# Kernel tuning notes

Measured on AMD Instinct MI355X. Metric: run time of the kernel, lower is better.

The kernel has to match this reference:

```python
import jax, jax.numpy as jnp
import numpy as np

B, ISIZE, HSIZE = 256, 256, 512
CLIPVAL = 2.0

def _linear(x, W, b):
    # torch nn.Linear: y = x @ W.T + b, W is [out, in]
    return x @ W.T + b

def setup_inputs() -> dict:
    key = jax.random.key(0)
    ks = jax.random.split(key, 24)
    d = {}
    d['inputs'] = jax.random.normal(ks[0], (B, ISIZE), jnp.float32)
    d['h0'] = jax.random.normal(ks[1], (B, HSIZE), jnp.float32) * 0.1
    d['c0'] = jax.random.normal(ks[2], (B, HSIZE), jnp.float32) * 0.1
    d['hebb'] = jax.random.normal(ks[3], (B, HSIZE, HSIZE), jnp.float32) * 0.01
    d['w'] = 0.02 * jax.random.uniform(ks[4], (HSIZE, HSIZE), jnp.float32) - 0.01
    d['alpha'] = 0.0001 * jax.random.uniform(ks[5], (1, 1, HSIZE), jnp.float32)
    scale_h = 1.0 / np.sqrt(HSIZE)
    scale_i = 1.0 / np.sqrt(ISIZE)
    d['h2f_w'] = jax.random.uniform(ks[6], (HSIZE, HSIZE), jnp.float32, -scale_h, scale_h)
    d['h2f_b'] = jax.random.uniform(ks[7], (HSIZE,), jnp.float32, -scale_h, scale_h)
    d['h2i_w'] = jax.random.uniform(ks[8], (HSIZE, HSIZE), jnp.float32, -scale_h, scale_h)
    d['h2i_b'] = jax.random.uniform(ks[9], (HSIZE,), jnp.float32, -scale_h, scale_h)
    d['h2opt_w'] = jax.random.uniform(ks[10], (HSIZE, HSIZE), jnp.float32, -scale_h, scale_h)
    d['h2opt_b'] = jax.random.uniform(ks[11], (HSIZE,), jnp.float32, -scale_h, scale_h)
    d['x2f_w'] = jax.random.uniform(ks[12], (HSIZE, ISIZE), jnp.float32, -scale_i, scale_i)
    d['x2f_b'] = jax.random.uniform(ks[13], (HSIZE,), jnp.float32, -scale_i, scale_i)
    d['x2i_w'] = jax.random.uniform(ks[14], (HSIZE, ISIZE), jnp.float32, -scale_i, scale_i)
    d['x2i_b'] = jax.random.uniform(ks[15], (HSIZE,), jnp.float32, -scale_i, scale_i)
    d['x2opt_w'] = jax.random.uniform(ks[16], (HSIZE, ISIZE), jnp.float32, -scale_i, scale_i)
    d['x2opt_b'] = jax.random.uniform(ks[17], (HSIZE,), jnp.float32, -scale_i, scale_i)
    d['x2c_w'] = jax.random.uniform(ks[18], (HSIZE, ISIZE), jnp.float32, -scale_i, scale_i)
    d['x2c_b'] = jax.random.uniform(ks[19], (HSIZE,), jnp.float32, -scale_i, scale_i)
    d['h2mod_w'] = jax.random.uniform(ks[20], (1, HSIZE), jnp.float32, -scale_h, scale_h)
    d['h2mod_b'] = jax.random.uniform(ks[21], (1,), jnp.float32, -scale_h, scale_h)
    d['modfanout_w'] = jax.random.uniform(ks[22], (HSIZE, 1), jnp.float32, -1.0, 1.0)
    d['modfanout_b'] = jax.random.uniform(ks[23], (HSIZE,), jnp.float32, -1.0, 1.0)
    return d

def reference(inputs, h0, c0, hebb, w, alpha,
              h2f_w, h2f_b, h2i_w, h2i_b, h2opt_w, h2opt_b,
              x2f_w, x2f_b, x2i_w, x2i_b, x2opt_w, x2opt_b, x2c_w, x2c_b,
              h2mod_w, h2mod_b, modfanout_w, modfanout_b):
    # gates
    fgt = jax.nn.sigmoid(_linear(inputs, x2f_w, x2f_b) + _linear(h0, h2f_w, h2f_b))
    ipt = jax.nn.sigmoid(_linear(inputs, x2i_w, x2i_b) + _linear(h0, h2i_w, h2i_b))
    opt = jax.nn.sigmoid(_linear(inputs, x2opt_w, x2opt_b) + _linear(h0, h2opt_w, h2opt_b))
    # plastic recurrent matmul: h [B,h] x (w + alpha*hebb) [B,h,h]
    M = w[None, :, :] + alpha * hebb  # [B, h, h]
    h2coutput = jnp.einsum('bh,bhk->bk', h0, M)
    inputstocell = jnp.tanh(_linear(inputs, x2c_w, x2c_b) + h2coutput)
    cell = fgt * c0 + ipt * inputstocell
    hactiv = opt * jnp.tanh(cell)
    # Hebbian outer product (hebboutput='i2c')
    deltahebb = h0[:, :, None] * inputstocell[:, None, :]  # [B, h, h]
    # modulation: modultype='modplasth2mod', modulout='fanout'
    m = jnp.tanh(_linear(hactiv, h2mod_w, h2mod_b))  # [B, 1]
    fan = m[:, 0][:, None] * modfanout_w[:, 0][None, :] + modfanout_b[None, :]  # [B, h]
    myeta = fan[:, None, :]  # [B, 1, h]
    # cliptype='clip'
    hebb_new = jnp.clip(hebb + myeta * deltahebb, -CLIPVAL, CLIPVAL)
    return hactiv, cell, hebb_new
```

## Files before the change

kernel.cpp:

```cpp
#include <hip/hip_runtime.h>
#include <math.h>

#define BATCH 256
#define ISZ 256
#define H 512
#define BH (BATCH * H)
#define CLIPV 2.0f

typedef float f4_t __attribute__((ext_vector_type(4)));

__device__ __forceinline__ float sigmoidf_(float x) { return 1.0f / (1.0f + expf(-x)); }
__device__ __forceinline__ f4_t nt_load4(const f4_t* p) { return __builtin_nontemporal_load(p); }
__device__ __forceinline__ void nt_store4(f4_t* p, f4_t v) { __builtin_nontemporal_store(v, p); }

#define BT 64
#define KT 32
#define LDSP (BT + 4)
#define NGEMM 256
#define NEIN  1024

__global__ __launch_bounds__(256) void gemms_einsum(
    const float* __restrict__ x, const float* __restrict__ h0,
    const float* __restrict__ x2f_w, const float* __restrict__ x2f_b,
    const float* __restrict__ h2f_w, const float* __restrict__ h2f_b,
    const float* __restrict__ x2i_w, const float* __restrict__ x2i_b,
    const float* __restrict__ h2i_w, const float* __restrict__ h2i_b,
    const float* __restrict__ x2o_w, const float* __restrict__ x2o_b,
    const float* __restrict__ h2o_w, const float* __restrict__ h2o_b,
    const float* __restrict__ x2c_w, const float* __restrict__ x2c_b,
    const float* __restrict__ w,
    const float* __restrict__ hebb,
    float* __restrict__ pre, float* __restrict__ hbpart)
{
  __shared__ __align__(16) float As[KT][LDSP];
  __shared__ __align__(16) float Bs[KT][LDSP];
  __shared__ float h0s[128];
  __shared__ f4_t redv[128];

  const int bid = blockIdx.x;
  const int t   = threadIdx.x;

  if (bid >= NGEMM) {
    const int e    = bid - NGEMM;
    const int b    = e >> 2;
    const int seg  = e & 3;
    const int col  = t & 127;
    const int half = t >> 7;
    if (t < 128) h0s[t] = h0[b * H + seg * 128 + t];
    __syncthreads();
    const f4_t* hb4 = (const f4_t*)hebb +
        (size_t)(b * H + seg * 128 + half * 64) * (H / 4) + col;
    f4_t acc = {0.f, 0.f, 0.f, 0.f};
    #pragma unroll 8
    for (int h = 0; h < 64; ++h) {
      acc += h0s[half * 64 + h] * hb4[(size_t)h * 128];
    }
    if (half == 1) redv[col] = acc;
    __syncthreads();
    if (half == 0) {
      acc += redv[col];
      ((f4_t*)hbpart)[(size_t)(b * 4 + seg) * 128 + col] = acc;
    }
    return;
  }

  const int ch  = bid >> 5;
  const int rem = bid & 31;
  const int n0  = (rem & 7) * BT;
  const int m0  = (rem >> 3) * BT;
  const int tx = t & 15, ty = t >> 4;

  const float* A; const float* Bm; int lda, K; bool kmajor = true;
  const float* b1 = nullptr; const float* b2 = nullptr;
  switch (ch) {
    case 0: A = x;  lda = ISZ; K = ISZ; Bm = x2f_w; b1 = x2f_b; b2 = h2f_b; break;
    case 1: A = h0; lda = H;   K = H;   Bm = h2f_w; break;
    case 2: A = x;  lda = ISZ; K = ISZ; Bm = x2i_w; b1 = x2i_b; b2 = h2i_b; break;
    case 3: A = h0; lda = H;   K = H;   Bm = h2i_w; break;
    case 4: A = x;  lda = ISZ; K = ISZ; Bm = x2o_w; b1 = x2o_b; b2 = h2o_b; break;
    case 5: A = h0; lda = H;   K = H;   Bm = h2o_w; break;
    case 6: A = x;  lda = ISZ; K = ISZ; Bm = x2c_w; b1 = x2c_b; break;
    default: A = h0; lda = H;  K = H;   Bm = w; kmajor = false; break;
  }

  float acc[4][4] = {{0.0f}};

  for (int kk0 = 0; kk0 < K; kk0 += KT) {
    #pragma unroll
    for (int i = 0; i < 2; ++i) {
      int l = i * 256 + t;
      int r = l >> 3, c = l & 7;
      float4 v = *(const float4*)&A[(size_t)(m0 + r) * lda + kk0 + c * 4];
      As[c * 4 + 0][r] = v.x; As[c * 4 + 1][r] = v.y;
      As[c * 4 + 2][r] = v.z; As[c * 4 + 3][r] = v.w;
    }
    if (kmajor) {
      #pragma unroll
      for (int i = 0; i < 2; ++i) {
        int l = i * 256 + t;
        int n = l >> 3, c = l & 7;
        float4 v = *(const float4*)&Bm[(size_t)(n0 + n) * K + kk0 + c * 4];
        Bs[c * 4 + 0][n] = v.x; Bs[c * 4 + 1][n] = v.y;
        Bs[c * 4 + 2][n] = v.z; Bs[c * 4 + 3][n] = v.w;
      }
    } else {
      #pragma unroll
      for (int i = 0; i < 2; ++i) {
        int l = i * 256 + t;
        int j = l >> 4, c = l & 15;
        float4 v = *(const float4*)&Bm[(size_t)(kk0 + j) * H + n0 + c * 4];
        *(float4*)&Bs[j][c * 4] = v;
      }
    }
    __syncthreads();
    #pragma unroll
    for (int j = 0; j < KT; ++j) {
      float4 a  = *(const float4*)&As[j][ty * 4];
      float4 bv = *(const float4*)&Bs[j][tx * 4];
      float av[4] = {a.x, a.y, a.z, a.w};
      float bw[4] = {bv.x, bv.y, bv.z, bv.w};
      #pragma unroll
      for (int r = 0; r < 4; ++r)
        #pragma unroll
        for (int c = 0; c < 4; ++c)
          acc[r][c] += av[r] * bw[c];
    }
    __syncthreads();
  }

  float bias[4];
  #pragma unroll
  for (int c = 0; c < 4; ++c) {
    int n = n0 + tx * 4 + c;
    float bv = 0.0f;
    if (b1) bv += b1[n];
    if (b2) bv += b2[n];
    bias[c] = bv;
  }
  float* outc = pre + (size_t)ch * BH;
  #pragma unroll
  for (int r = 0; r < 4; ++r) {
    int m = m0 + ty * 4 + r;
    float4 o;
    o.x = acc[r][0] + bias[0];
    o.y = acc[r][1] + bias[1];
    o.z = acc[r][2] + bias[2];
    o.w = acc[r][3] + bias[3];
    *(float4*)&outc[(size_t)m * H + n0 + tx * 4] = o;
  }
}

__global__ __launch_bounds__(256) void fuse_mod(
    const float* __restrict__ pre, const float* __restrict__ hbpart,
    const float* __restrict__ c0, const float* __restrict__ alpha,
    const float* __restrict__ h2mod_w, const float* __restrict__ h2mod_b,
    const float* __restrict__ mfo_w, const float* __restrict__ mfo_b,
    float* __restrict__ out, float* __restrict__ eta)
{
  const int b = blockIdx.x, t = threadIdx.x;
  float ha[2], itcv[2];
  #pragma unroll
  for (int u = 0; u < 2; ++u) {
    const int k   = t + u * 256;
    const int idx = b * H + k;
    float hb = 0.0f;
    #pragma unroll
    for (int s = 0; s < 4; ++s) hb += hbpart[(size_t)(b * 4 + s) * H + k];
    float h2c = pre[(size_t)7 * BH + idx] + alpha[k] * hb;
    float it  = tanhf(pre[(size_t)6 * BH + idx] + h2c);
    float f = sigmoidf_(pre[idx]                + pre[(size_t)1 * BH + idx]);
    float i = sigmoidf_(pre[(size_t)2 * BH + idx] + pre[(size_t)3 * BH + idx]);
    float o = sigmoidf_(pre[(size_t)4 * BH + idx] + pre[(size_t)5 * BH + idx]);
    float cell = f * c0[idx] + i * it;
    float h = o * tanhf(cell);
    out[idx] = h;
    out[BH + idx] = cell;
    ha[u] = h; itcv[u] = it;
  }
  float s = ha[0] * h2mod_w[t] + ha[1] * h2mod_w[t + 256];
  #pragma unroll
  for (int off = 32; off > 0; off >>= 1) s += __shfl_down(s, off, 64);
  __shared__ float red[4];
  __shared__ float mm;
  if ((t & 63) == 0) red[t >> 6] = s;
  __syncthreads();
  if (t == 0) mm = tanhf(red[0] + red[1] + red[2] + red[3] + h2mod_b[0]);
  __syncthreads();
  float m = mm;
  #pragma unroll
  for (int u = 0; u < 2; ++u) {
    const int k = t + u * 256;
    eta[b * H + k] = (m * mfo_w[k] + mfo_b[k]) * itcv[u];
  }
}

__global__ __launch_bounds__(256) void hebb_update(
    const float* __restrict__ hebb, const float* __restrict__ h0,
    const float* __restrict__ eta, float* __restrict__ out)
{
  const size_t g = (size_t)(gridDim.x - 1 - blockIdx.x) * 256 + threadIdx.x;
  f4_t v = nt_load4((const f4_t*)hebb + g);
  const int k4  = (int)(g & 127);
  const int row = (int)(g >> 7);
  const int b   = row >> 9;
  f4_t e = ((const f4_t*)eta)[(b << 7) + k4];
  float s = h0[row];
  f4_t r;
  r.x = fminf(fmaxf(v.x + s * e.x, -CLIPV), CLIPV);
  r.y = fminf(fmaxf(v.y + s * e.y, -CLIPV), CLIPV);
  r.z = fminf(fmaxf(v.z + s * e.z, -CLIPV), CLIPV);
  r.w = fminf(fmaxf(v.w + s * e.w, -CLIPV), CLIPV);
  nt_store4((f4_t*)out + (size_t)(2 * BH / 4) + g, r);
}

extern "C" void kernel_launch(void* const* d_in, const int* in_sizes, int n_in,
                              void* d_out, int out_size, void* d_ws, size_t ws_size,
                              hipStream_t stream) {
  const float* x       = (const float*)d_in[0];
  const float* h0      = (const float*)d_in[1];
  const float* c0      = (const float*)d_in[2];
  const float* hebb    = (const float*)d_in[3];
  const float* w       = (const float*)d_in[4];
  const float* alpha   = (const float*)d_in[5];
  const float* h2f_w   = (const float*)d_in[6];
  const float* h2f_b   = (const float*)d_in[7];
  const float* h2i_w   = (const float*)d_in[8];
  const float* h2i_b   = (const float*)d_in[9];
  const float* h2o_w   = (const float*)d_in[10];
  const float* h2o_b   = (const float*)d_in[11];
  const float* x2f_w   = (const float*)d_in[12];
  const float* x2f_b   = (const float*)d_in[13];
  const float* x2i_w   = (const float*)d_in[14];
  const float* x2i_b   = (const float*)d_in[15];
  const float* x2o_w   = (const float*)d_in[16];
  const float* x2o_b   = (const float*)d_in[17];
  const float* x2c_w   = (const float*)d_in[18];
  const float* x2c_b   = (const float*)d_in[19];
  const float* h2mod_w = (const float*)d_in[20];
  const float* h2mod_b = (const float*)d_in[21];
  const float* mfo_w   = (const float*)d_in[22];
  const float* mfo_b   = (const float*)d_in[23];

  float* out = (float*)d_out;
  float* ws  = (float*)d_ws;

  float* pre    = ws;
  float* hbpart = pre + (size_t)8 * BH;
  float* eta    = hbpart + (size_t)BATCH * 4 * H;

  gemms_einsum<<<NGEMM + NEIN, 256, 0, stream>>>(
      x, h0, x2f_w, x2f_b, h2f_w, h2f_b, x2i_w, x2i_b, h2i_w, h2i_b,
      x2o_w, x2o_b, h2o_w, h2o_b, x2c_w, x2c_b, w, hebb, pre, hbpart);

  fuse_mod<<<BATCH, 256, 0, stream>>>(
      pre, hbpart, c0, alpha, h2mod_w, h2mod_b, mfo_w, mfo_b, out, eta);

  hebb_update<<<(BH * (H / 4)) / 256, 256, 0, stream>>>(hebb, h0, eta, out);
}
```

Baseline: 541.1 us.

## Fuse hebb einsum, gate math and hebb update into one per-batch kernel

Moves the plastic einsum out of the GEMM kernel into a per-batch kernel that computes h0·hebb, the gate nonlinearities, the modulation and the clipped Hebbian update in one launch. The aim is to reread each batch's 1 MB hebb slice right after reducing over it, so the second read may hit L2/MALL instead of HBM, and to drop the hbpart and eta workspace round trips plus one launch. The cost is only 256 blocks of 512 threads doing all of the 256 MB hebb traffic, so there may not be enough bytes in flight to saturate HBM bandwidth. The einsum also no longer overlaps with the GEMM blocks.

```diff
diff --git a/kernel.cpp b/kernel.cpp
--- a/kernel.cpp
+++ b/kernel.cpp
@@ -7,19 +7,16 @@
 #define BH (BATCH * H)
 #define CLIPV 2.0f
 
-typedef float f4_t __attribute__((ext_vector_type(4)));
-
-__device__ __forceinline__ float sigmoidf_(float x) { return 1.0f / (1.0f + expf(-x)); }
-__device__ __forceinline__ f4_t nt_load4(const f4_t* p) { return __builtin_nontemporal_load(p); }
-__device__ __forceinline__ void nt_store4(f4_t* p, f4_t v) { __builtin_nontemporal_store(v, p); }
-
 #define BT 64
 #define KT 32
 #define LDSP (BT + 4)
-#define NGEMM 256
-#define NEIN  1024
-
-__global__ __launch_bounds__(256) void gemms_einsum(
+
+typedef float f4_t __attribute__((ext_vector_type(4)));
+
+__device__ __forceinline__ float sigmoidf_(float x) { return 1.0f / (1.0f + expf(-x)); }
+__device__ __forceinline__ void nt_store4(f4_t* p, f4_t v) { __builtin_nontemporal_store(v, p); }
+
+__global__ __launch_bounds__(256) void gemms(
     const float* __restrict__ x, const float* __restrict__ h0,
     const float* __restrict__ x2f_w, const float* __restrict__ x2f_b,
     const float* __restrict__ h2f_w, const float* __restrict__ h2f_b,
@@ -29,41 +26,13 @@
     const float* __restrict__ h2o_w, const float* __restrict__ h2o_b,
     const float* __restrict__ x2c_w, const float* __restrict__ x2c_b,
     const float* __restrict__ w,
-    const float* __restrict__ hebb,
-    float* __restrict__ pre, float* __restrict__ hbpart)
+    float* __restrict__ pre)
 {
   __shared__ __align__(16) float As[KT][LDSP];
   __shared__ __align__(16) float Bs[KT][LDSP];
-  __shared__ float h0s[128];
-  __shared__ f4_t redv[128];
 
   const int bid = blockIdx.x;
   const int t   = threadIdx.x;
-
-  if (bid >= NGEMM) {
-    const int e    = bid - NGEMM;
-    const int b    = e >> 2;
-    const int seg  = e & 3;
-    const int col  = t & 127;
-    const int half = t >> 7;
-    if (t < 128) h0s[t] = h0[b * H + seg * 128 + t];
-    __syncthreads();
-    const f4_t* hb4 = (const f4_t*)hebb +
-        (size_t)(b * H + seg * 128 + half * 64) * (H / 4) + col;
-    f4_t acc = {0.f, 0.f, 0.f, 0.f};
-    #pragma unroll 8
-    for (int h = 0; h < 64; ++h) {
-      acc += h0s[half * 64 + h] * hb4[(size_t)h * 128];
-    }
-    if (half == 1) redv[col] = acc;
-    __syncthreads();
-    if (half == 0) {
-      acc += redv[col];
-      ((f4_t*)hbpart)[(size_t)(b * 4 + seg) * 128 + col] = acc;
-    }
-    return;
-  }
-
   const int ch  = bid >> 5;
   const int rem = bid & 31;
   const int n0  = (rem & 7) * BT;
@@ -84,7 +53,6 @@
   }
 
   float acc[4][4] = {{0.0f}};
-
   for (int kk0 = 0; kk0 < K; kk0 += KT) {
     #pragma unroll
     for (int i = 0; i < 2; ++i) {
@@ -150,67 +118,79 @@
   }
 }
 
-__global__ __launch_bounds__(256) void fuse_mod(
-    const float* __restrict__ pre, const float* __restrict__ hbpart,
-    const float* __restrict__ c0, const float* __restrict__ alpha,
+__global__ __launch_bounds__(512) void batch_fused(
+    const float* __restrict__ pre, const float* __restrict__ hebb,
+    const float* __restrict__ h0, const float* __restrict__ c0,
+    const float* __restrict__ alpha,
     const float* __restrict__ h2mod_w, const float* __restrict__ h2mod_b,
     const float* __restrict__ mfo_w, const float* __restrict__ mfo_b,
-    float* __restrict__ out, float* __restrict__ eta)
+    float* __restrict__ out)
 {
-  const int b = blockIdx.x, t = threadIdx.x;
-  float ha[2], itcv[2];
-  #pragma unroll
-  for (int u = 0; u < 2; ++u) {
-    const int k   = t + u * 256;
-    const int idx = b * H + k;
-    float hb = 0.0f;
-    #pragma unroll
-    for (int s = 0; s < 4; ++s) hb += hbpart[(size_t)(b * 4 + s) * H + k];
-    float h2c = pre[(size_t)7 * BH + idx] + alpha[k] * hb;
-    float it  = tanhf(pre[(size_t)6 * BH + idx] + h2c);
-    float f = sigmoidf_(pre[idx]                + pre[(size_t)1 * BH + idx]);
-    float i = sigmoidf_(pre[(size_t)2 * BH + idx] + pre[(size_t)3 * BH + idx]);
-    float o = sigmoidf_(pre[(size_t)4 * BH + idx] + pre[(size_t)5 * BH + idx]);
-    float cell = f * c0[idx] + i * it;
-    float h = o * tanhf(cell);
-    out[idx] = h;
-    out[BH + idx] = cell;
-    ha[u] = h; itcv[u] = it;
-  }
-  float s = ha[0] * h2mod_w[t] + ha[1] * h2mod_w[t + 256];
+  __shared__ float h0s[H];
+  __shared__ f4_t redv[3][128];
+  __shared__ float hbs[H];
+  __shared__ float red[8];
+  __shared__ float mm;
+  __shared__ f4_t eta4[128];
+
+  const int b   = blockIdx.x;
+  const int t   = threadIdx.x;
+  const int col = t & 127;
+  const int rg  = t >> 7;
+
+  h0s[t] = h0[b * H + t];
+  __syncthreads();
+
+  const f4_t* hb4 = (const f4_t*)hebb + ((size_t)b * H + rg * 128) * 128 + col;
+  f4_t acc = {0.f, 0.f, 0.f, 0.f};
+  #pragma unroll 8
+  for (int h = 0; h < 128; ++h)
+    acc += h0s[rg * 128 + h] * hb4[(size_t)h * 128];
+  if (rg) redv[rg - 1][col] = acc;
+  __syncthreads();
+  if (rg == 0) {
+    acc += redv[0][col]; acc += redv[1][col]; acc += redv[2][col];
+    *(f4_t*)&hbs[col * 4] = acc;
+  }
+  __syncthreads();
+
+  const size_t idx = (size_t)b * H + t;
+  float h2c  = pre[(size_t)7 * BH + idx] + alpha[t] * hbs[t];
+  float itcv = tanhf(pre[(size_t)6 * BH + idx] + h2c);
+  float f = sigmoidf_(pre[idx]                  + pre[(size_t)1 * BH + idx]);
+  float i = sigmoidf_(pre[(size_t)2 * BH + idx] + pre[(size_t)3 * BH + idx]);
+  float o = sigmoidf_(pre[(size_t)4 * BH + idx] + pre[(size_t)5 * BH + idx]);
+  float cell = f * c0[idx] + i * itcv;
+  float hav  = o * tanhf(cell);
+  out[idx] = hav;
+  out[BH + idx] = cell;
+
+  float s = hav * h2mod_w[t];
   #pragma unroll
   for (int off = 32; off > 0; off >>= 1) s += __shfl_down(s, off, 64);
-  __shared__ float red[4];
-  __shared__ float mm;
   if ((t & 63) == 0) red[t >> 6] = s;
   __syncthreads();
-  if (t == 0) mm = tanhf(red[0] + red[1] + red[2] + red[3] + h2mod_b[0]);
-  __syncthreads();
-  float m = mm;
-  #pragma unroll
-  for (int u = 0; u < 2; ++u) {
-    const int k = t + u * 256;
-    eta[b * H + k] = (m * mfo_w[k] + mfo_b[k]) * itcv[u];
-  }
-}
-
-__global__ __launch_bounds__(256) void hebb_update(
-    const float* __restrict__ hebb, const float* __restrict__ h0,
-    const float* __restrict__ eta, float* __restrict__ out)
-{
-  const size_t g = (size_t)(gridDim.x - 1 - blockIdx.x) * 256 + threadIdx.x;
-  f4_t v = nt_load4((const f4_t*)hebb + g);
-  const int k4  = (int)(g & 127);
-  const int row = (int)(g >> 7);
-  const int b   = row >> 9;
-  f4_t e = ((const f4_t*)eta)[(b << 7) + k4];
-  float s = h0[row];
-  f4_t r;
-  r.x = fminf(fmaxf(v.x + s * e.x, -CLIPV), CLIPV);
-  r.y = fminf(fmaxf(v.y + s * e.y, -CLIPV), CLIPV);
-  r.z = fminf(fmaxf(v.z + s * e.z, -CLIPV), CLIPV);
-  r.w = fminf(fmaxf(v.w + s * e.w, -CLIPV), CLIPV);
-  nt_store4((f4_t*)out + (size_t)(2 * BH / 4) + g, r);
+  if (t == 0)
+    mm = tanhf(red[0] + red[1] + red[2] + red[3] +
+               red[4] + red[5] + red[6] + red[7] + h2mod_b[0]);
+  __syncthreads();
+  ((float*)eta4)[t] = (mm * mfo_w[t] + mfo_b[t]) * itcv;
+  __syncthreads();
+
+  f4_t e = eta4[col];
+  f4_t* dst = (f4_t*)out + (size_t)(2 * BH / 4) +
+              ((size_t)b * H + rg * 128) * 128 + col;
+  #pragma unroll 8
+  for (int h = 127; h >= 0; --h) {
+    float sh = h0s[rg * 128 + h];
+    f4_t v = hb4[(size_t)h * 128];
+    f4_t r;
+    r.x = fminf(fmaxf(v.x + sh * e.x, -CLIPV), CLIPV);
+    r.y = fminf(fmaxf(v.y + sh * e.y, -CLIPV), CLIPV);
+    r.z = fminf(fmaxf(v.z + sh * e.z, -CLIPV), CLIPV);
+    r.w = fminf(fmaxf(v.w + sh * e.w, -CLIPV), CLIPV);
+    nt_store4(dst + (size_t)h * 128, r);
+  }
 }
 
 extern "C" void kernel_launch(void* const* d_in, const int* in_sizes, int n_in,
@@ -242,18 +222,12 @@
   const float* mfo_b   = (const float*)d_in[23];
 
   float* out = (float*)d_out;
-  float* ws  = (float*)d_ws;
-
-  float* pre    = ws;
-  float* hbpart = pre + (size_t)8 * BH;
-  float* eta    = hbpart + (size_t)BATCH * 4 * H;
-
-  gemms_einsum<<<NGEMM + NEIN, 256, 0, stream>>>(
+  float* pre = (float*)d_ws;
+
+  gemms<<<256, 256, 0, stream>>>(
       x, h0, x2f_w, x2f_b, h2f_w, h2f_b, x2i_w, x2i_b, h2i_w, h2i_b,
-      x2o_w, x2o_b, h2o_w, h2o_b, x2c_w, x2c_b, w, hebb, pre, hbpart);
-
-  fuse_mod<<<BATCH, 256, 0, stream>>>(
-      pre, hbpart, c0, alpha, h2mod_w, h2mod_b, mfo_w, mfo_b, out, eta);
-
-  hebb_update<<<(BH * (H / 4)) / 256, 256, 0, stream>>>(hebb, h0, eta, out);
+      x2o_w, x2o_b, h2o_w, h2o_b, x2c_w, x2c_b, w, pre);
+
+  batch_fused<<<BATCH, 512, 0, stream>>>(
+      pre, hebb, h0, c0, alpha, h2mod_w, h2mod_b, mfo_w, mfo_b, out);
 }
```

After: 559.3 us. 3.4% more time.
